# Kernel optimization log

Hardware: AMD Instinct MI355X
Metric: run time of the kernel (lower is better)

Reference implementation:

```python
import jax, jax.numpy as jnp
import numpy as np
import math

H = 12          # num_attention_heads
DH = 64         # attention_head_size
D = H * DH      # hidden_size = 768
LN_EPS = 1e-5
GAUSS_W = 0.3989422804014327
WIDS = [None, 0.1, 1.0, 5.0]


def gauss_weight(L, wid):
    # faithful to generate_gauss_weight: row-normalized Gaussian bump per query pos
    center = (jnp.arange(L, dtype=jnp.float32) / L)[:, None]       # (L,1)
    pos = jnp.linspace(0.0, 1.0, L, dtype=jnp.float32)[None, :]    # (1,L)
    width = max(wid, 0.01) / 9.0                                   # static python scalar
    g = (GAUSS_W / width) * jnp.exp(-(pos - center) ** 2 / (2.0 * width * width))
    return g / jnp.max(g, axis=-1, keepdims=True)                  # (L,L)


def layer_norm(x, g, b):
    mu = jnp.mean(x, axis=-1, keepdims=True)
    var = jnp.mean((x - mu) ** 2, axis=-1, keepdims=True)
    return (x - mu) * jax.lax.rsqrt(var + LN_EPS) * g + b


def bert_attention(x, mask, qkv_w, qkv_b, out_w, out_b, ln_g, ln_b, wid):
    # x: (N,L,D); mask: (N,L,L); qkv_w: (3,D,D); qkv_b: (3,D)
    N, L, _ = x.shape

    def heads(t):  # (N,L,D) -> (N,H,L,DH)
        return t.reshape(N, L, H, DH).transpose(0, 2, 1, 3)

    q = heads(x @ qkv_w[0] + qkv_b[0])
    k = heads(x @ qkv_w[1] + qkv_b[1])
    v = heads(x @ qkv_w[2] + qkv_b[2])

    scores = jnp.einsum('nhqd,nhkd->nhqk', q, k) / math.sqrt(DH)   # (N,H,L,L)
    if wid is not None:
        scores = scores * gauss_weight(L, wid)[None, None]          # multiplicative GMM mask
    scores = scores + (1.0 - mask[:, None, :, :]) * -10000.0
    probs = jax.nn.softmax(scores, axis=-1)                         # dropout = identity (eval)
    ctx = jnp.einsum('nhqk,nhkd->nhqd', probs, v)                   # (N,H,L,DH)
    ctx = ctx.transpose(0, 2, 1, 3).reshape(N, L, D)

    proj = ctx @ out_w + out_b
    return layer_norm(proj + x, ln_g, ln_b)


def setup_inputs() -> dict:
    key = jax.random.key(0)
    ks = jax.random.split(key, 4)
    N, L = 4, 1024
    s = 0.02
    return {
        'input_tensor': jax.random.normal(ks[0], (N, L, D), dtype=jnp.float32),
        'attention_mask': jnp.ones((N, L, L), dtype=jnp.float32),
        'qkv_w': jax.random.normal(ks[1], (4, 3, D, D), dtype=jnp.float32) * s,
        'qkv_b': jnp.zeros((4, 3, D), dtype=jnp.float32),
        'out_w': jax.random.normal(ks[2], (4, D, D), dtype=jnp.float32) * s,
        'out_b': jnp.zeros((4, D), dtype=jnp.float32),
        'ln_g': jnp.ones((4, D), dtype=jnp.float32),
        'ln_b': jnp.zeros((4, D), dtype=jnp.float32),
    }


def reference(input_tensor, attention_mask, qkv_w, qkv_b, out_w, out_b, ln_g, ln_b):
    # pure_block=False path: 4 parallel GMM-masked attention branches, averaged
    outs = [
        bert_attention(input_tensor, attention_mask,
                       qkv_w[i], qkv_b[i], out_w[i], out_b[i], ln_g[i], ln_b[i], WIDS[i])
        for i in range(4)
    ]
    return jnp.mean(jnp.stack(outs, axis=-1), axis=-1)
```

## Files before the change

kernel.cpp:

```cpp
#include <hip/hip_runtime.h>
#include <hip/hip_bf16.h>

#define NB 4
#define LQ 1024
#define NH 12
#define DHD 64
#define DM 768
#define MTOT (NB*LQ)
#define L2E 1.4426950408889634f
#define SMB 11.541560327111708f
#define CFAR 3.3546262790251185e-4f

typedef __attribute__((ext_vector_type(4))) float f32x4;
typedef __attribute__((ext_vector_type(8))) short bf16x8;
typedef __attribute__((ext_vector_type(4))) short short4v;
typedef unsigned short u16;

#if __has_builtin(__builtin_amdgcn_exp2f)
#define EXP2(x) __builtin_amdgcn_exp2f(x)
#else
#define EXP2(x) __expf((x) * 0.6931471805599453f)
#endif

__device__ __forceinline__ u16 f2bf(float f){
  union { float f; unsigned int i; } v; v.f = f;
  unsigned int r = v.i + 0x7FFFu + ((v.i >> 16) & 1u);
  return (u16)(r >> 16);
}
__device__ __forceinline__ float bf2f(u16 u){
  union { unsigned int i; float f; } v; v.i = ((unsigned int)u) << 16;
  return v.f;
}
__device__ __forceinline__ unsigned cvt_pk_bf16(float lo, float hi){
  unsigned r;
  asm("v_cvt_pk_bf16_f32 %0, %1, %2" : "=v"(r) : "v"(lo), "v"(hi));
  return r;
}

typedef const __attribute__((address_space(1))) void* gas_t;
typedef __attribute__((address_space(3))) void* las_t;
__device__ __forceinline__ void gload16(const void* g, void* l){
  __builtin_amdgcn_global_load_lds((gas_t)g, (las_t)l, 16, 0, 0);
}

__global__ void k_cvt_x(const float* __restrict__ x, u16* __restrict__ xb){
  int i = (blockIdx.x * 256 + threadIdx.x) * 4;
  float4 v = *reinterpret_cast<const float4*>(x + i);
  short4v o;
  o[0] = (short)f2bf(v.x); o[1] = (short)f2bf(v.y);
  o[2] = (short)f2bf(v.z); o[3] = (short)f2bf(v.w);
  *reinterpret_cast<short4v*>(xb + i) = o;
}

__global__ void k_wt(const float* __restrict__ qkv_w, const float* __restrict__ out_w,
                     u16* __restrict__ wt){
  int mat = blockIdx.z;
  const float* W = (mat < 12) ? (qkv_w + (size_t)mat*DM*DM)
                              : (out_w + (size_t)(mat-12)*DM*DM);
  __shared__ float tile[32][33];
  int j0 = blockIdx.x*32, k0 = blockIdx.y*32;
  int tx = threadIdx.x, ty = threadIdx.y;
  #pragma unroll
  for (int i=0;i<4;i++)
    tile[ty + i*8][tx] = W[(size_t)(k0 + ty + i*8)*DM + j0 + tx];
  __syncthreads();
  u16* dst = wt + (size_t)mat*DM*DM;
  #pragma unroll
  for (int i=0;i<4;i++)
    dst[(size_t)(j0 + ty + i*8)*DM + k0 + tx] = f2bf(tile[tx][ty + i*8]);
}

__global__ void k_maskchk(const float* __restrict__ mask, unsigned* __restrict__ flags){
  int qt = blockIdx.x, kt = blockIdx.y, n = blockIdx.z;
  const float* M = mask + ((size_t)(n*LQ) + qt*64)*LQ + kt*64;
  int tid = threadIdx.x;
  int r = tid >> 2, c4 = (tid & 3) * 16;
  int ok = 1;
  #pragma unroll
  for (int j=0;j<4;j++){
    float4 v = *reinterpret_cast<const float4*>(M + (size_t)r*LQ + c4 + j*4);
    ok &= (v.x==1.f) & (v.y==1.f) & (v.z==1.f) & (v.w==1.f);
  }
  __shared__ int sok[4];
  unsigned long long bal = __ballot(ok);
  if ((tid & 63) == 0) sok[tid>>6] = (bal == 0xFFFFFFFFFFFFFFFFull) ? 1 : 0;
  __syncthreads();
  if (tid == 0) flags[((size_t)n*16 + qt)*16 + kt] = sok[0] & sok[1] & sok[2] & sok[3];
}

__global__ __launch_bounds__(256) void k_vsum(const u16* __restrict__ qkvws, float* __restrict__ ps){
  const int nh = blockIdx.x;
  const int b  = blockIdx.y;
  const size_t blk = (size_t)NB*NH*LQ*DHD;
  const u16* Vt = qkvws + (size_t)(b*3+2)*blk + (size_t)nh*DHD*LQ;
  const int tid = threadIdx.x;
  const int dh = tid >> 2, c = tid & 3;
  float* psb = ps + ((size_t)(b*48 + nh)*17)*64;
  float acc = 0.f;
  for (int kt = 0; kt < 16; ++kt){
    if (c == 0) psb[kt*64 + dh] = acc;
    bf16x8 v0 = *reinterpret_cast<const bf16x8*>(&Vt[(size_t)dh*LQ + kt*64 + c*16]);
    bf16x8 v1 = *reinterpret_cast<const bf16x8*>(&Vt[(size_t)dh*LQ + kt*64 + c*16 + 8]);
    float s = 0.f;
    #pragma unroll
    for (int j=0;j<8;j++) s += bf2f((u16)v0[j]) + bf2f((u16)v1[j]);
    s += __shfl_xor(s, 1);
    s += __shfl_xor(s, 2);
    acc += s;
  }
  if (c == 0) psb[16*64 + dh] = acc;
}

__device__ __forceinline__ void gemm_tile(const u16* __restrict__ Ag,
                                          const u16* __restrict__ Bg,
                                          u16* a_lds, u16* b_lds, f32x4 acc[4][4])
{
  const int tid = threadIdx.x, lane = tid & 63, w = tid >> 6;
  const int wr = (w >> 1) * 64, wc = (w & 1) * 64;
  const int rl = lane & 15, q4 = lane >> 4;
  const int lrow = lane >> 3;
  const int lseg = (lane & 7) ^ lrow;
  for (int k0 = 0; k0 < DM; k0 += 64) {
    __syncthreads();
    #pragma unroll
    for (int cc = 0; cc < 4; ++cc) {
      int c = w*4 + cc;
      const u16* ga = Ag + (size_t)(c*8 + lrow)*DM + k0 + lseg*8;
      const u16* gb = Bg + (size_t)(c*8 + lrow)*DM + k0 + lseg*8;
      gload16(ga, a_lds + c*512);
      gload16(gb, b_lds + c*512);
    }
    __syncthreads();
    #pragma unroll
    for (int half = 0; half < 2; ++half) {
      bf16x8 af[4], bfr[4];
      #pragma unroll
      for (int f = 0; f < 4; ++f) {
        int ra = wr + f*16 + rl;
        int rb = wc + f*16 + rl;
        int ta = (half*4 + q4) ^ (ra & 7);
        int tb = (half*4 + q4) ^ (rb & 7);
        af[f]  = *reinterpret_cast<const bf16x8*>(&a_lds[ra*64 + ta*8]);
        bfr[f] = *reinterpret_cast<const bf16x8*>(&b_lds[rb*64 + tb*8]);
      }
      #pragma unroll
      for (int mf=0; mf<4; ++mf)
        #pragma unroll
        for (int nf=0; nf<4; ++nf)
          acc[mf][nf] = __builtin_amdgcn_mfma_f32_16x16x32_bf16(af[mf], bfr[nf], acc[mf][nf], 0,0,0);
    }
  }
}

__global__ __launch_bounds__(256) void k_qkv(const u16* __restrict__ xb, const u16* __restrict__ wt,
                     const float* __restrict__ qkv_b, u16* __restrict__ qkvws)
{
  __shared__ __align__(16) u16 a_lds[128*64];
  __shared__ __align__(16) u16 b_lds[128*64];
  const int bid = blockIdx.x;
  const int orig = (bid & 7) * 288 + (bid >> 3);
  const int m0 = (orig & 31) * 128;
  const int j0 = ((orig >> 5) % 6) * 128;
  const int mat = orig / 192;
  const int t = mat % 3;
  f32x4 acc[4][4] = {};
  gemm_tile(xb + (size_t)m0*DM, wt + (size_t)mat*DM*DM + (size_t)j0*DM, a_lds, b_lds, acc);

  const int tid = threadIdx.x, lane = tid & 63, w = tid >> 6;
  const int wr = (w >> 1) * 64, wc = (w & 1) * 64;
  const int rl = lane & 15, rg = (lane >> 4) * 4;
  const float sc = (t == 0) ? 0.125f : 1.0f;
  const size_t matbase = (size_t)mat * ((size_t)NB*NH*LQ*DHD);
  #pragma unroll
  for (int nf=0; nf<4; ++nf) {
    int j = j0 + wc + nf*16 + rl;
    float bias = qkv_b[mat*DM + j];
    int h = j >> 6, dh = j & 63;
    #pragma unroll
    for (int mf=0; mf<4; ++mf) {
      int mB = m0 + wr + mf*16 + rg;
      int n = mB >> 10, l = mB & 1023;
      if (t < 2) {
        #pragma unroll
        for (int i=0;i<4;i++)
          qkvws[matbase + ((size_t)(n*NH + h)*LQ + (l+i))*DHD + dh] = f2bf((acc[mf][nf][i] + bias) * sc);
      } else {
        short4v pk;
        #pragma unroll
        for (int i=0;i<4;i++) pk[i] = (short)f2bf(acc[mf][nf][i] + bias);
        *reinterpret_cast<short4v*>(&qkvws[matbase + ((size_t)(n*NH + h)*DHD + dh)*LQ + l]) = pk;
      }
    }
  }
}

__global__ __launch_bounds__(256) void k_attn(const u16* __restrict__ qkvws, const float* __restrict__ mask,
                      const unsigned* __restrict__ flags, const float* __restrict__ ps,
                      u16* __restrict__ ctx, float c2_1, float c2_2, float c2_3)
{
  __shared__ __align__(16) u16 kv_lds[2][2][64*64];
  __shared__ __align__(16) u16 p_lds[64*64];
  const int bid = blockIdx.x;
  const int orig = (bid & 7) * 384 + (bid >> 3);
  const int qt = orig & 15;
  const int b  = (orig >> 4) & 3;
  const int nh = orig >> 6;
  const int n = nh / NH, h = nh % NH;
  const float c2 = (b==1) ? c2_1 : (b==2) ? c2_2 : c2_3;
  const bool useG = (b != 0);
  const int tid = threadIdx.x, lane = tid & 63, w = tid >> 6;
  const int rl = lane & 15, q4 = lane >> 4, kc8 = q4*8, rg = q4*4;

  const size_t hb = (size_t)(n*NH + h);
  const size_t blk = (size_t)NB*NH*LQ*DHD;
  const u16* Qb = qkvws + (size_t)(b*3+0)*blk + hb*LQ*DHD;
  const u16* Kb = qkvws + (size_t)(b*3+1)*blk + hb*LQ*DHD;
  const u16* Vt = qkvws + (size_t)(b*3+2)*blk + hb*DHD*LQ;
  const float* Mb = mask + (size_t)n*LQ*LQ;

  const int q0 = qt*64;
  const int qrow = q0 + w*16 + rl;
  bf16x8 qf0 = *reinterpret_cast<const bf16x8*>(&Qb[(size_t)qrow*DHD + kc8]);
  bf16x8 qf1 = *reinterpret_cast<const bf16x8*>(&Qb[(size_t)qrow*DHD + 32 + kc8]);

  float srun[4] = {0.f,0.f,0.f,0.f};
  float dmin2[4], cq[4];
  f32x4 o[4] = {};
  #pragma unroll
  for (int i=0;i<4;i++){
    int q = q0 + w*16 + rg + i;
    float c = (float)q * (1.0f/1024.0f);
    float tq = c * 1023.0f;
    float ksf = floorf(tq + 0.5f);
    float dm = ksf * (1.0f/1023.0f) - c;
    cq[i] = c; dmin2[i] = dm*dm;
  }

  int rowall = 1;
  for (int t = 0; t < 16; ++t) rowall &= (flags[((size_t)n*16 + qt)*16 + t] != 0u) ? 1 : 0;

  int ktlo = 0, kthi = 16;
  if (rowall){
    if (b == 1){ ktlo = qt > 0 ? qt-1 : 0; kthi = qt < 15 ? qt+2 : 16; }
    else if (b == 2){ ktlo = qt > 5 ? qt-5 : 0; kthi = qt < 10 ? qt+6 : 16; }
  }
  const int nt = kthi - ktlo;

  if (rowall && nt < 16){
    const float* psb = ps + ((size_t)(b*48 + nh)*17)*64;
    #pragma unroll
    for (int nf=0; nf<4; ++nf){
      int dh = nf*16 + rl;
      float sfar = psb[16*64 + dh] - psb[kthi*64 + dh] + psb[ktlo*64 + dh];
      float fv = CFAR * sfar;
      #pragma unroll
      for (int i=0;i<4;i++) o[nf][i] = fv;
    }
    float sinit = CFAR * (float)(64*(16 - nt));
    #pragma unroll
    for (int i=0;i<4;i++) srun[i] = sinit;
  }

  const int l8 = lane >> 3, srcu = (lane & 7) ^ l8;

  #define STAGE(buf, kt_) { \
    _Pragma("unroll") \
    for (int cc=0; cc<2; ++cc){ \
      int c = w*2 + cc; \
      gload16(Kb + (size_t)((kt_)*64 + c*8 + l8)*DHD + srcu*8, (u16*)kv_lds[buf][0] + c*512); \
      gload16(Vt + (size_t)(c*8 + l8)*LQ + (kt_)*64 + srcu*8, (u16*)kv_lds[buf][1] + c*512); \
    } }

  STAGE(0, ktlo);
  __syncthreads();

  for (int it = 0; it < nt; ++it){
    const int kt = ktlo + it;
    const int cur = it & 1;
    if (it + 1 < nt) STAGE(cur^1, kt+1);
    const bool allones = rowall || (flags[((size_t)n*16 + qt)*16 + kt] != 0u);
    const u16* kbuf = (const u16*)kv_lds[cur][0];
    const u16* vbuf = (const u16*)kv_lds[cur][1];

    f32x4 sf[4] = {};
    #pragma unroll
    for (int nf=0; nf<4; ++nf){
      int row = nf*16 + rl, sw = (row & 7) << 3;
      bf16x8 kf0 = *reinterpret_cast<const bf16x8*>(&kbuf[row*64 + (kc8 ^ sw)]);
      bf16x8 kf1 = *reinterpret_cast<const bf16x8*>(&kbuf[row*64 + ((32 + kc8) ^ sw)]);
      sf[nf] = __builtin_amdgcn_mfma_f32_16x16x32_bf16(qf0, kf0, sf[nf], 0,0,0);
      sf[nf] = __builtin_amdgcn_mfma_f32_16x16x32_bf16(qf1, kf1, sf[nf], 0,0,0);
    }

    float pv[4][4];
    #pragma unroll
    for (int nf=0; nf<4; ++nf){
      int key = kt*64 + nf*16 + rl;
      float pos = (float)key * (1.0f/1023.0f);
      #pragma unroll
      for (int i=0;i<4;i++){
        float s = sf[nf][i];
        if (useG){
          float d = pos - cq[i];
          float tg = fmaf(-d, d, dmin2[i]);
          s *= EXP2(tg * c2);
        }
        if (!allones){
          int q = q0 + w*16 + rg + i;
          s = fmaf(1.0f - Mb[(size_t)q*LQ + key], -10000.0f, s);
        }
        float p = EXP2(fmaf(s, L2E, -SMB));
        srun[i] += p;
        pv[nf][i] = p;
      }
    }

    #pragma unroll
    for (int np=0; np<2; ++np)
      #pragma unroll
      for (int i=0;i<4;i++){
        unsigned u = cvt_pk_bf16(pv[np*2][i], pv[np*2+1][i]);
        int row = w*16 + rg + i, sw = (row & 7) << 3;
        p_lds[row*64 + ((np*32 + rl) ^ sw)]      = (u16)(u & 0xffffu);
        p_lds[row*64 + ((np*32 + 16 + rl) ^ sw)] = (u16)(u >> 16);
      }
    asm volatile("s_waitcnt lgkmcnt(0)" ::: "memory");
    __builtin_amdgcn_sched_barrier(0);

    {
      int prow = w*16 + rl, psw = (prow & 7) << 3;
      bf16x8 pa0 = *reinterpret_cast<const bf16x8*>(&p_lds[prow*64 + (kc8 ^ psw)]);
      bf16x8 pa1 = *reinterpret_cast<const bf16x8*>(&p_lds[prow*64 + ((32 + kc8) ^ psw)]);
      #pragma unroll
      for (int nf=0; nf<4; ++nf){
        int row = nf*16 + rl, sw = (row & 7) << 3;
        bf16x8 vb0 = *reinterpret_cast<const bf16x8*>(&vbuf[row*64 + (kc8 ^ sw)]);
        bf16x8 vb1 = *reinterpret_cast<const bf16x8*>(&vbuf[row*64 + ((32 + kc8) ^ sw)]);
        o[nf] = __builtin_amdgcn_mfma_f32_16x16x32_bf16(pa0, vb0, o[nf], 0,0,0);
        o[nf] = __builtin_amdgcn_mfma_f32_16x16x32_bf16(pa1, vb1, o[nf], 0,0,0);
      }
    }
    __syncthreads();
  }

  #pragma unroll
  for (int off=1; off<16; off<<=1){
    #pragma unroll
    for (int i=0;i<4;i++) srun[i] += __shfl_xor(srun[i], off);
  }
  #pragma unroll
  for (int i=0;i<4;i++){
    float inv = 1.0f / (srun[i] + 1e-35f);
    int q = q0 + w*16 + rg + i;
    size_t mrow = ((size_t)(n*LQ + q)) * DM;
    #pragma unroll
    for (int nf=0; nf<4; ++nf){
      int d = h*DHD + nf*16 + rl;
      ctx[(size_t)b*((size_t)MTOT*DM) + mrow + d] = f2bf(o[nf][i] * inv);
    }
  }
}

__global__ __launch_bounds__(256) void k_proj(const u16* __restrict__ ctx, const u16* __restrict__ wt,
                      const float* __restrict__ out_b, u16* __restrict__ proj)
{
  __shared__ __align__(16) u16 a_lds[128*64];
  __shared__ __align__(16) u16 b_lds[128*64];
  const int bid = blockIdx.x;
  const int orig = (bid & 7) * 96 + (bid >> 3);
  const int m0 = (orig & 31) * 128;
  const int j0 = ((orig >> 5) % 6) * 128;
  const int b = orig / 192;
  f32x4 acc[4][4] = {};
  gemm_tile(ctx + (size_t)b*MTOT*DM + (size_t)m0*DM,
            wt + (size_t)(12+b)*DM*DM + (size_t)j0*DM, a_lds, b_lds, acc);
  const int tid = threadIdx.x, lane = tid & 63, w = tid >> 6;
  const int wr = (w >> 1) * 64, wc = (w & 1) * 64;
  const int rl = lane & 15, rg = (lane >> 4) * 4;
  #pragma unroll
  for (int nf=0; nf<4; ++nf) {
    int j = j0 + wc + nf*16 + rl;
    float bias = out_b[b*DM + j];
    #pragma unroll
    for (int mf=0; mf<4; ++mf) {
      int mB = m0 + wr + mf*16 + rg;
      #pragma unroll
      for (int i=0;i<4;i++)
        proj[((size_t)b*MTOT + (mB+i))*DM + j] = f2bf(acc[mf][nf][i] + bias);
    }
  }
}

__global__ __launch_bounds__(256) void k_ln(const float* __restrict__ x, const u16* __restrict__ proj,
                    const float* __restrict__ ln_g, const float* __restrict__ ln_b,
                    float* __restrict__ out)
{
  const int m = blockIdx.x;
  const int tid = threadIdx.x, lane = tid & 63, w = tid >> 6;
  __shared__ float rb[2][4];
  float xr[3], acc[3] = {0.f,0.f,0.f};
  #pragma unroll
  for (int c=0;c<3;c++) xr[c] = x[(size_t)m*DM + tid + c*256];
  for (int b=0;b<4;b++){
    float v[3]; float s1 = 0.f, s2 = 0.f;
    #pragma unroll
    for (int c=0;c<3;c++){
      v[c] = bf2f(proj[((size_t)b*MTOT + m)*DM + tid + c*256]) + xr[c];
      s1 += v[c]; s2 += v[c]*v[c];
    }
    #pragma unroll
    for (int off=32; off>=1; off>>=1){
      s1 += __shfl_xor(s1, off);
      s2 += __shfl_xor(s2, off);
    }
    if (lane == 0){ rb[0][w] = s1; rb[1][w] = s2; }
    __syncthreads();
    s1 = rb[0][0]+rb[0][1]+rb[0][2]+rb[0][3];
    s2 = rb[1][0]+rb[1][1]+rb[1][2]+rb[1][3];
    __syncthreads();
    float mu = s1 * (1.0f/768.0f);
    float var = s2 * (1.0f/768.0f) - mu*mu;
    float rs = rsqrtf(var + 1e-5f);
    #pragma unroll
    for (int c=0;c<3;c++){
      int j = tid + c*256;
      acc[c] += 0.25f * ((v[c]-mu)*rs*ln_g[b*DM+j] + ln_b[b*DM+j]);
    }
  }
  #pragma unroll
  for (int c=0;c<3;c++) out[(size_t)m*DM + tid + c*256] = acc[c];
}

extern "C" void kernel_launch(void* const* d_in, const int* in_sizes, int n_in,
                              void* d_out, int out_size, void* d_ws, size_t ws_size,
                              hipStream_t stream)
{
  const float* x     = (const float*)d_in[0];
  const float* mask  = (const float*)d_in[1];
  const float* qkv_w = (const float*)d_in[2];
  const float* qkv_b = (const float*)d_in[3];
  const float* out_w = (const float*)d_in[4];
  const float* out_b = (const float*)d_in[5];
  const float* ln_g  = (const float*)d_in[6];
  const float* ln_b  = (const float*)d_in[7];
  float* out = (float*)d_out;
  char* ws = (char*)d_ws;

  u16* xb        = (u16*)(ws);
  unsigned* flags= (unsigned*)(ws);
  float* ps      = (float*)(ws + 8192);
  u16* wt        = (u16*)(ws + 6291456);
  u16* qkv       = (u16*)(ws + 25165824);
  u16* ctx       = (u16*)(ws + 100663296);
  u16* proj      = (u16*)(ws + 25165824);

  float c2[3];
  const float wid[3] = {0.1f, 1.0f, 5.0f};
  for (int i=0;i<3;i++){
    float wdt = wid[i]/9.0f;
    c2[i] = (1.0f/(2.0f*wdt*wdt)) * L2E;
  }

  k_cvt_x<<<dim3(3072), dim3(256), 0, stream>>>(x, xb);
  k_wt<<<dim3(24,24,16), dim3(32,8), 0, stream>>>(qkv_w, out_w, wt);
  k_qkv<<<dim3(2304), dim3(256), 0, stream>>>(xb, wt, qkv_b, qkv);
  k_vsum<<<dim3(48,4), dim3(256), 0, stream>>>(qkv, ps);
  k_maskchk<<<dim3(16,16,4), dim3(256), 0, stream>>>(mask, flags);
  k_attn<<<dim3(3072), dim3(256), 0, stream>>>(qkv, mask, flags, ps, ctx, c2[0], c2[1], c2[2]);
  k_proj<<<dim3(768), dim3(256), 0, stream>>>(ctx, wt, out_b, proj);
  k_ln<<<dim3(4096), dim3(256), 0, stream>>>(x, proj, ln_g, ln_b, out);
}
```

Baseline: 270.8 us.

## Load K/V fragments directly from global, vectorize weight transpose, batch LN reductions

The attention kernel drops its double-buffered LDS staging of K and V tiles and the per-iteration barrier. Each wave now reads its MFMA K and V fragments straight from global memory, relying on L2 and L1 caching, and declares launch bounds of 3 blocks per SM for higher occupancy. The weight transpose kernel now packs four bf16 values per store, and the layernorm kernel computes all four branch reductions before a single barrier instead of two barriers per branch. The risk is that global-memory latency is no longer hidden by the async prefetch, and each wave reloads the same K/V data.

```diff
diff --git a/kernel.cpp b/kernel.cpp
--- a/kernel.cpp
+++ b/kernel.cpp
@@ -65,9 +65,12 @@
     tile[ty + i*8][tx] = W[(size_t)(k0 + ty + i*8)*DM + j0 + tx];
   __syncthreads();
   u16* dst = wt + (size_t)mat*DM*DM;
-  #pragma unroll
-  for (int i=0;i<4;i++)
-    dst[(size_t)(j0 + ty + i*8)*DM + k0 + tx] = f2bf(tile[tx][ty + i*8]);
+  int tid = ty*32 + tx;
+  int jj = tid >> 3, kq = tid & 7;
+  short4v pk;
+  #pragma unroll
+  for (int t=0;t<4;t++) pk[t] = (short)f2bf(tile[kq*4 + t][jj]);
+  *reinterpret_cast<short4v*>(&dst[(size_t)(j0 + jj)*DM + k0 + kq*4]) = pk;
 }
 
 __global__ void k_maskchk(const float* __restrict__ mask, unsigned* __restrict__ flags){
@@ -194,11 +197,10 @@
   }
 }
 
-__global__ __launch_bounds__(256) void k_attn(const u16* __restrict__ qkvws, const float* __restrict__ mask,
+__global__ __launch_bounds__(256, 3) void k_attn(const u16* __restrict__ qkvws, const float* __restrict__ mask,
                       const unsigned* __restrict__ flags, const float* __restrict__ ps,
                       u16* __restrict__ ctx, float c2_1, float c2_2, float c2_3)
 {
-  __shared__ __align__(16) u16 kv_lds[2][2][64*64];
   __shared__ __align__(16) u16 p_lds[64*64];
   const int bid = blockIdx.x;
   const int orig = (bid & 7) * 384 + (bid >> 3);
@@ -261,33 +263,23 @@
     for (int i=0;i<4;i++) srun[i] = sinit;
   }
 
-  const int l8 = lane >> 3, srcu = (lane & 7) ^ l8;
-
-  #define STAGE(buf, kt_) { \
-    _Pragma("unroll") \
-    for (int cc=0; cc<2; ++cc){ \
-      int c = w*2 + cc; \
-      gload16(Kb + (size_t)((kt_)*64 + c*8 + l8)*DHD + srcu*8, (u16*)kv_lds[buf][0] + c*512); \
-      gload16(Vt + (size_t)(c*8 + l8)*LQ + (kt_)*64 + srcu*8, (u16*)kv_lds[buf][1] + c*512); \
-    } }
-
-  STAGE(0, ktlo);
-  __syncthreads();
-
   for (int it = 0; it < nt; ++it){
     const int kt = ktlo + it;
-    const int cur = it & 1;
-    if (it + 1 < nt) STAGE(cur^1, kt+1);
     const bool allones = rowall || (flags[((size_t)n*16 + qt)*16 + kt] != 0u);
-    const u16* kbuf = (const u16*)kv_lds[cur][0];
-    const u16* vbuf = (const u16*)kv_lds[cur][1];
+    const u16* kp = Kb + (size_t)(kt*64)*DHD;
+
+    bf16x8 vb0[4], vb1[4];
+    #pragma unroll
+    for (int nf=0; nf<4; ++nf){
+      vb0[nf] = *reinterpret_cast<const bf16x8*>(&Vt[(size_t)(nf*16+rl)*LQ + kt*64 + kc8]);
+      vb1[nf] = *reinterpret_cast<const bf16x8*>(&Vt[(size_t)(nf*16+rl)*LQ + kt*64 + 32 + kc8]);
+    }
 
     f32x4 sf[4] = {};
     #pragma unroll
     for (int nf=0; nf<4; ++nf){
-      int row = nf*16 + rl, sw = (row & 7) << 3;
-      bf16x8 kf0 = *reinterpret_cast<const bf16x8*>(&kbuf[row*64 + (kc8 ^ sw)]);
-      bf16x8 kf1 = *reinterpret_cast<const bf16x8*>(&kbuf[row*64 + ((32 + kc8) ^ sw)]);
+      bf16x8 kf0 = *reinterpret_cast<const bf16x8*>(&kp[(nf*16+rl)*DHD + kc8]);
+      bf16x8 kf1 = *reinterpret_cast<const bf16x8*>(&kp[(nf*16+rl)*DHD + 32 + kc8]);
       sf[nf] = __builtin_amdgcn_mfma_f32_16x16x32_bf16(qf0, kf0, sf[nf], 0,0,0);
       sf[nf] = __builtin_amdgcn_mfma_f32_16x16x32_bf16(qf1, kf1, sf[nf], 0,0,0);
     }
@@ -333,14 +325,10 @@
       bf16x8 pa1 = *reinterpret_cast<const bf16x8*>(&p_lds[prow*64 + ((32 + kc8) ^ psw)]);
       #pragma unroll
       for (int nf=0; nf<4; ++nf){
-        int row = nf*16 + rl, sw = (row & 7) << 3;
-        bf16x8 vb0 = *reinterpret_cast<const bf16x8*>(&vbuf[row*64 + (kc8 ^ sw)]);
-        bf16x8 vb1 = *reinterpret_cast<const bf16x8*>(&vbuf[row*64 + ((32 + kc8) ^ sw)]);
-        o[nf] = __builtin_amdgcn_mfma_f32_16x16x32_bf16(pa0, vb0, o[nf], 0,0,0);
-        o[nf] = __builtin_amdgcn_mfma_f32_16x16x32_bf16(pa1, vb1, o[nf], 0,0,0);
+        o[nf] = __builtin_amdgcn_mfma_f32_16x16x32_bf16(pa0, vb0[nf], o[nf], 0,0,0);
+        o[nf] = __builtin_amdgcn_mfma_f32_16x16x32_bf16(pa1, vb1[nf], o[nf], 0,0,0);
       }
     }
-    __syncthreads();
   }
 
   #pragma unroll
@@ -397,34 +385,41 @@
 {
   const int m = blockIdx.x;
   const int tid = threadIdx.x, lane = tid & 63, w = tid >> 6;
-  __shared__ float rb[2][4];
+  __shared__ float rb[4][2][4];
   float xr[3], acc[3] = {0.f,0.f,0.f};
   #pragma unroll
   for (int c=0;c<3;c++) xr[c] = x[(size_t)m*DM + tid + c*256];
+  float vv[4][3], s1[4], s2[4];
+  #pragma unroll
   for (int b=0;b<4;b++){
-    float v[3]; float s1 = 0.f, s2 = 0.f;
+    s1[b] = 0.f; s2[b] = 0.f;
     #pragma unroll
     for (int c=0;c<3;c++){
-      v[c] = bf2f(proj[((size_t)b*MTOT + m)*DM + tid + c*256]) + xr[c];
-      s1 += v[c]; s2 += v[c]*v[c];
-    }
+      float v = bf2f(proj[((size_t)b*MTOT + m)*DM + tid + c*256]) + xr[c];
+      vv[b][c] = v; s1[b] += v; s2[b] += v*v;
+    }
+  }
+  #pragma unroll
+  for (int b=0;b<4;b++){
     #pragma unroll
     for (int off=32; off>=1; off>>=1){
-      s1 += __shfl_xor(s1, off);
-      s2 += __shfl_xor(s2, off);
-    }
-    if (lane == 0){ rb[0][w] = s1; rb[1][w] = s2; }
-    __syncthreads();
-    s1 = rb[0][0]+rb[0][1]+rb[0][2]+rb[0][3];
-    s2 = rb[1][0]+rb[1][1]+rb[1][2]+rb[1][3];
-    __syncthreads();
-    float mu = s1 * (1.0f/768.0f);
-    float var = s2 * (1.0f/768.0f) - mu*mu;
+      s1[b] += __shfl_xor(s1[b], off);
+      s2[b] += __shfl_xor(s2[b], off);
+    }
+    if (lane == 0){ rb[b][0][w] = s1[b]; rb[b][1][w] = s2[b]; }
+  }
+  __syncthreads();
+  #pragma unroll
+  for (int b=0;b<4;b++){
+    float S1 = rb[b][0][0]+rb[b][0][1]+rb[b][0][2]+rb[b][0][3];
+    float S2 = rb[b][1][0]+rb[b][1][1]+rb[b][1][2]+rb[b][1][3];
+    float mu = S1 * (1.0f/768.0f);
+    float var = S2 * (1.0f/768.0f) - mu*mu;
     float rs = rsqrtf(var + 1e-5f);
     #pragma unroll
     for (int c=0;c<3;c++){
       int j = tid + c*256;
-      acc[c] += 0.25f * ((v[c]-mu)*rs*ln_g[b*DM+j] + ln_b[b*DM+j]);
+      acc[c] += 0.25f * ((vv[b][c]-mu)*rs*ln_g[b*DM+j] + ln_b[b*DM+j]);
     }
   }
   #pragma unroll
```

New measurement: 445.6 us. 64.6% more time.
